# Kernel optimization log

Measured on AMD Instinct MI355X. Metric: run time of the kernel, lower is better.

## Reference

```python
import jax, jax.numpy as jnp
import numpy as np

R = 7            # radius
STRIDE = 2       # downsample_factor
K_SIDE = 2 * R + 1   # 15 -> K = 225 neighbors


def setup_inputs() -> dict:
    key = jax.random.key(0)
    B, H, W = 8, 512, 512
    # integer segment labels in [0, 64), stored as float32
    segments = jax.random.randint(key, (B, 1, H, W), 0, 64).astype(jnp.float32)
    return {"segments": segments}


def _local_equality_adj(segments):
    # segments: [B, 1, H_full, W_full]
    seg = segments[..., ::STRIDE, ::STRIDE]          # [B, 1, H, W]
    B, _, H, W = seg.shape
    x = seg[:, 0]                                    # [B, H, W]
    # zero-pad borders by R (unfold-style neighborhood extraction)
    padded = jnp.pad(x, ((0, 0), (R, R), (R, R)))    # [B, H+2R, W+2R]
    offs = jnp.arange(K_SIDE)
    dy, dx = jnp.meshgrid(offs, offs, indexing="ij")
    dy = dy.reshape(-1)                              # [K]
    dx = dx.reshape(-1)                              # [K]

    def gather(dy_i, dx_i):
        return jax.lax.dynamic_slice(padded, (0, dy_i, dx_i), (B, H, W))

    neighbors = jax.vmap(gather)(dy, dx)             # [K, B, H, W]
    neighbors = jnp.transpose(neighbors, (1, 0, 2, 3))  # [B, K, H, W]
    # broadcast equality: center [B,1,H,W] vs neighbors [B,K,H,W]
    adj = (seg == neighbors).astype(jnp.float32)     # [B, K, H, W]
    return adj


def reference(segments):
    return _local_equality_adj(segments)
```

## Files before the change

### kernel.cpp

```cpp
#include <hip/hip_runtime.h>


#define RAD 7
#define KS 15
#define HW 256
#define IN_W 512
#define TILE_W (HW + 2 * RAD)
#define TILE_PITCH 272
#define PLANE (HW * HW)

typedef float vf4 __attribute__((ext_vector_type(4)));

__global__ __launch_bounds__(256) void adj_kernel(const float* __restrict__ in,
                                                  float* __restrict__ out) {
    __shared__ float smem[KS][TILE_PITCH];

    const int y   = blockIdx.x;
    const int b   = blockIdx.y;
    const int tid = threadIdx.x;

    const float* inb = in + (size_t)b * (IN_W * IN_W);

    #pragma unroll
    for (int r = 0; r < KS; ++r) {
        const int gy = y - RAD + r;
        for (int c = tid; c < TILE_PITCH; c += 256) {
            const int gx = c - RAD;
            float v = 0.0f;
            if ((unsigned)gy < HW && (unsigned)gx < HW) {
                v = inb[(size_t)(2 * gy) * IN_W + 2 * gx];
            }
            smem[r][c] = v;
        }
    }
    __syncthreads();

    const int wv   = tid >> 6;
    const int lane = tid & 63;
    const int x    = lane * 4;

    const float s0 = smem[RAD][x + RAD + 0];
    const float s1 = smem[RAD][x + RAD + 1];
    const float s2 = smem[RAD][x + RAD + 2];
    const float s3 = smem[RAD][x + RAD + 3];

    float* base = out + (size_t)b * (KS * KS * (size_t)PLANE) + (size_t)y * HW + x;

    for (int r = wv; r < KS; r += 4) {
        const float* rowp = &smem[r][x];
        vf4 w0 = *(const vf4*)(rowp + 0);
        vf4 w1 = *(const vf4*)(rowp + 4);
        vf4 w2 = *(const vf4*)(rowp + 8);
        vf4 w3 = *(const vf4*)(rowp + 12);
        vf4 w4 = *(const vf4*)(rowp + 16);
        float win[20] = { w0.x, w0.y, w0.z, w0.w,
                          w1.x, w1.y, w1.z, w1.w,
                          w2.x, w2.y, w2.z, w2.w,
                          w3.x, w3.y, w3.z, w3.w,
                          w4.x, w4.y, w4.z, w4.w };
        float* op = base + (size_t)(r * KS) * PLANE;
        #pragma unroll
        for (int dc = 0; dc < KS; ++dc) {
            vf4 v;
            v.x = (s0 == win[dc + 0]) ? 1.0f : 0.0f;
            v.y = (s1 == win[dc + 1]) ? 1.0f : 0.0f;
            v.z = (s2 == win[dc + 2]) ? 1.0f : 0.0f;
            v.w = (s3 == win[dc + 3]) ? 1.0f : 0.0f;
            __builtin_nontemporal_store(v, (vf4*)op);
            op += PLANE;
        }
    }
}

extern "C" void kernel_launch(void* const* d_in, const int* in_sizes, int n_in,
                              void* d_out, int out_size, void* d_ws, size_t ws_size,
                              hipStream_t stream) {
    const float* segments = (const float*)d_in[0];
    float* out = (float*)d_out;
    dim3 grid(HW, 8);
    dim3 block(256);
    adj_kernel<<<grid, block, 0, stream>>>(segments, out);
}
```

Before: 463.0 us.

## Split into padded downsample pass and per-plane output-contiguous comparison kernel

```diff
diff --git a/kernel.cpp b/kernel.cpp
--- a/kernel.cpp
+++ b/kernel.cpp
@@ -5,70 +5,100 @@
 #define KS 15
 #define HW 256
 #define IN_W 512
-#define TILE_W (HW + 2 * RAD)
-#define TILE_PITCH 272
 #define PLANE (HW * HW)
+#define WSROWS 270
+#define WSPITCH 272
+#define WSPLANE (WSROWS * WSPITCH)
+#define WS_BYTES ((size_t)8 * WSPLANE * 4)
 
 typedef float vf4 __attribute__((ext_vector_type(4)));
 
-__global__ __launch_bounds__(256) void adj_kernel(const float* __restrict__ in,
+__global__ __launch_bounds__(256) void downsample_pad(const float* __restrict__ in,
+                                                      float* __restrict__ ws) {
+    int t = blockIdx.x * 256 + threadIdx.x;
+    const int N = 8 * WSPLANE;
+    if (t >= N) return;
+    int xx   = t % WSPITCH;
+    int rest = t / WSPITCH;
+    int yy   = rest % WSROWS;
+    int b    = rest / WSROWS;
+    int gy = yy - RAD;
+    int gx = xx - 8;
+    float v = 0.0f;
+    if ((unsigned)gy < HW && (unsigned)gx < HW) {
+        v = in[(size_t)b * (IN_W * IN_W) + (size_t)(2 * gy) * IN_W + 2 * gx];
+    }
+    ws[t] = v;
+}
+
+__global__ __launch_bounds__(256) void adj_planes(const float* __restrict__ ws,
                                                   float* __restrict__ out) {
-    __shared__ float smem[KS][TILE_PITCH];
+    const int bx = blockIdx.x;
+    const int p  = bx >> 2;
+    const int y0 = (bx & 3) * 64;
+    const int b  = blockIdx.y;
+    const int dy = p / KS;
+    const int dx = p - dy * KS;
 
-    const int y   = blockIdx.x;
-    const int b   = blockIdx.y;
-    const int tid = threadIdx.x;
-
-    const float* inb = in + (size_t)b * (IN_W * IN_W);
-
-    #pragma unroll
-    for (int r = 0; r < KS; ++r) {
-        const int gy = y - RAD + r;
-        for (int c = tid; c < TILE_PITCH; c += 256) {
-            const int gx = c - RAD;
-            float v = 0.0f;
-            if ((unsigned)gy < HW && (unsigned)gx < HW) {
-                v = inb[(size_t)(2 * gy) * IN_W + 2 * gx];
-            }
-            smem[r][c] = v;
-        }
-    }
-    __syncthreads();
-
+    const int tid  = threadIdx.x;
     const int wv   = tid >> 6;
     const int lane = tid & 63;
     const int x    = lane * 4;
 
-    const float s0 = smem[RAD][x + RAD + 0];
-    const float s1 = smem[RAD][x + RAD + 1];
-    const float s2 = smem[RAD][x + RAD + 2];
-    const float s3 = smem[RAD][x + RAD + 3];
+    const float* wsb = ws + (size_t)b * WSPLANE;
+    float* ob = out + ((size_t)(b * (KS * KS) + p)) * PLANE
+                    + (size_t)y0 * HW + x;
 
-    float* base = out + (size_t)b * (KS * KS * (size_t)PLANE) + (size_t)y * HW + x;
+    for (int yi = wv; yi < 64; yi += 4) {
+        const int y = y0 + yi;
+        const vf4 own = *(const vf4*)(wsb + (size_t)(y + RAD) * WSPITCH + 8 + x);
+        const float* np = wsb + (size_t)(y + dy) * WSPITCH + (x + dx + 1);
+        const float n0 = np[0], n1 = np[1], n2 = np[2], n3 = np[3];
+        vf4 v;
+        v.x = (own.x == n0) ? 1.0f : 0.0f;
+        v.y = (own.y == n1) ? 1.0f : 0.0f;
+        v.z = (own.z == n2) ? 1.0f : 0.0f;
+        v.w = (own.w == n3) ? 1.0f : 0.0f;
+        __builtin_nontemporal_store(v, (vf4*)(ob + (size_t)yi * HW));
+    }
+}
 
-    for (int r = wv; r < KS; r += 4) {
-        const float* rowp = &smem[r][x];
-        vf4 w0 = *(const vf4*)(rowp + 0);
-        vf4 w1 = *(const vf4*)(rowp + 4);
-        vf4 w2 = *(const vf4*)(rowp + 8);
-        vf4 w3 = *(const vf4*)(rowp + 12);
-        vf4 w4 = *(const vf4*)(rowp + 16);
-        float win[20] = { w0.x, w0.y, w0.z, w0.w,
-                          w1.x, w1.y, w1.z, w1.w,
-                          w2.x, w2.y, w2.z, w2.w,
-                          w3.x, w3.y, w3.z, w3.w,
-                          w4.x, w4.y, w4.z, w4.w };
-        float* op = base + (size_t)(r * KS) * PLANE;
+__global__ __launch_bounds__(256) void adj_planes_direct(const float* __restrict__ in,
+                                                         float* __restrict__ out) {
+    const int bx = blockIdx.x;
+    const int p  = bx >> 2;
+    const int y0 = (bx & 3) * 64;
+    const int b  = blockIdx.y;
+    const int dy = p / KS;
+    const int dx = p - dy * KS;
+
+    const int tid  = threadIdx.x;
+    const int wv   = tid >> 6;
+    const int lane = tid & 63;
+    const int x    = lane * 4;
+
+    const float* inb = in + (size_t)b * (IN_W * IN_W);
+    float* ob = out + ((size_t)(b * (KS * KS) + p)) * PLANE
+                    + (size_t)y0 * HW + x;
+
+    for (int yi = wv; yi < 64; yi += 4) {
+        const int y  = y0 + yi;
+        const int ny = y + dy - RAD;
+        const bool yok = (unsigned)ny < HW;
+        const float* own_row = inb + (size_t)(2 * y) * IN_W;
+        const float* nb_row  = inb + (size_t)(2 * (yok ? ny : 0)) * IN_W;
+        vf4 v;
         #pragma unroll
-        for (int dc = 0; dc < KS; ++dc) {
-            vf4 v;
-            v.x = (s0 == win[dc + 0]) ? 1.0f : 0.0f;
-            v.y = (s1 == win[dc + 1]) ? 1.0f : 0.0f;
-            v.z = (s2 == win[dc + 2]) ? 1.0f : 0.0f;
-            v.w = (s3 == win[dc + 3]) ? 1.0f : 0.0f;
-            __builtin_nontemporal_store(v, (vf4*)op);
-            op += PLANE;
+        for (int k = 0; k < 4; ++k) {
+            const float s = own_row[2 * (x + k)];
+            const int nx = x + k + dx - RAD;
+            float n = 0.0f;
+            if (yok && (unsigned)nx < HW) n = nb_row[2 * nx];
+            const float r = (s == n) ? 1.0f : 0.0f;
+            if (k == 0) v.x = r; else if (k == 1) v.y = r;
+            else if (k == 2) v.z = r; else v.w = r;
         }
+        __builtin_nontemporal_store(v, (vf4*)(ob + (size_t)yi * HW));
     }
 }
 
@@ -77,7 +107,13 @@
                               hipStream_t stream) {
     const float* segments = (const float*)d_in[0];
     float* out = (float*)d_out;
-    dim3 grid(HW, 8);
-    dim3 block(256);
-    adj_kernel<<<grid, block, 0, stream>>>(segments, out);
+
+    if (d_ws != nullptr && ws_size >= WS_BYTES) {
+        float* ws = (float*)d_ws;
+        const int N = 8 * WSPLANE;
+        downsample_pad<<<dim3((N + 255) / 256), dim3(256), 0, stream>>>(segments, ws);
+        adj_planes<<<dim3(KS * KS * 4, 8), dim3(256), 0, stream>>>(ws, out);
+    } else {
+        adj_planes_direct<<<dim3(KS * KS * 4, 8), dim3(256), 0, stream>>>(segments, out);
+    }
 }
```

After: 463.9 us. About the same (+0.2%).

## Parallelize over neighbor offsets with direct global reads instead of shared-memory tile

Applied to the files above, without the earlier changes.

```diff
diff --git a/kernel.cpp b/kernel.cpp
--- a/kernel.cpp
+++ b/kernel.cpp
@@ -5,70 +5,55 @@
 #define KS 15
 #define HW 256
 #define IN_W 512
-#define TILE_W (HW + 2 * RAD)
-#define TILE_PITCH 272
 #define PLANE (HW * HW)
 
 typedef float vf4 __attribute__((ext_vector_type(4)));
 
-__global__ __launch_bounds__(256) void adj_kernel(const float* __restrict__ in,
+__global__ __launch_bounds__(256) void adj_direct(const float* __restrict__ in,
                                                   float* __restrict__ out) {
-    __shared__ float smem[KS][TILE_PITCH];
+    const int p  = blockIdx.x;
+    const int y0 = blockIdx.y * 64;
+    const int b  = blockIdx.z;
+    const int dy = p / KS;
+    const int dx = p - dy * KS;
 
-    const int y   = blockIdx.x;
-    const int b   = blockIdx.y;
-    const int tid = threadIdx.x;
-
-    const float* inb = in + (size_t)b * (IN_W * IN_W);
-
-    #pragma unroll
-    for (int r = 0; r < KS; ++r) {
-        const int gy = y - RAD + r;
-        for (int c = tid; c < TILE_PITCH; c += 256) {
-            const int gx = c - RAD;
-            float v = 0.0f;
-            if ((unsigned)gy < HW && (unsigned)gx < HW) {
-                v = inb[(size_t)(2 * gy) * IN_W + 2 * gx];
-            }
-            smem[r][c] = v;
-        }
-    }
-    __syncthreads();
-
+    const int tid  = threadIdx.x;
     const int wv   = tid >> 6;
     const int lane = tid & 63;
     const int x    = lane * 4;
 
-    const float s0 = smem[RAD][x + RAD + 0];
-    const float s1 = smem[RAD][x + RAD + 1];
-    const float s2 = smem[RAD][x + RAD + 2];
-    const float s3 = smem[RAD][x + RAD + 3];
+    const float* inb = in + (size_t)b * (IN_W * IN_W);
+    float* ob = out + ((size_t)(b * (KS * KS) + p)) * PLANE
+                    + (size_t)y0 * HW + x;
 
-    float* base = out + (size_t)b * (KS * KS * (size_t)PLANE) + (size_t)y * HW + x;
+    const int nx0 = x + dx - RAD;
 
-    for (int r = wv; r < KS; r += 4) {
-        const float* rowp = &smem[r][x];
-        vf4 w0 = *(const vf4*)(rowp + 0);
-        vf4 w1 = *(const vf4*)(rowp + 4);
-        vf4 w2 = *(const vf4*)(rowp + 8);
-        vf4 w3 = *(const vf4*)(rowp + 12);
-        vf4 w4 = *(const vf4*)(rowp + 16);
-        float win[20] = { w0.x, w0.y, w0.z, w0.w,
-                          w1.x, w1.y, w1.z, w1.w,
-                          w2.x, w2.y, w2.z, w2.w,
-                          w3.x, w3.y, w3.z, w3.w,
-                          w4.x, w4.y, w4.z, w4.w };
-        float* op = base + (size_t)(r * KS) * PLANE;
+    for (int yi = wv; yi < 64; yi += 4) {
+        const int y  = y0 + yi;
+        const int ny = y + dy - RAD;
+        const bool yok = (unsigned)ny < (unsigned)HW;
+
+        const float* orow = inb + (size_t)(2 * y) * IN_W + 2 * x;
+        const vf4 o0 = *(const vf4*)(orow);
+        const vf4 o1 = *(const vf4*)(orow + 4);
+        const float s0 = o0.x, s1 = o0.z, s2 = o1.x, s3 = o1.z;
+
+        const float* nrow = inb + (size_t)(2 * (yok ? ny : 0)) * IN_W;
+        float n[4];
         #pragma unroll
-        for (int dc = 0; dc < KS; ++dc) {
-            vf4 v;
-            v.x = (s0 == win[dc + 0]) ? 1.0f : 0.0f;
-            v.y = (s1 == win[dc + 1]) ? 1.0f : 0.0f;
-            v.z = (s2 == win[dc + 2]) ? 1.0f : 0.0f;
-            v.w = (s3 == win[dc + 3]) ? 1.0f : 0.0f;
-            __builtin_nontemporal_store(v, (vf4*)op);
-            op += PLANE;
+        for (int k = 0; k < 4; ++k) {
+            const int c  = nx0 + k;
+            const bool ok = yok && ((unsigned)c < (unsigned)HW);
+            const float v = nrow[ok ? 2 * c : 0];
+            n[k] = ok ? v : 0.0f;
         }
+
+        vf4 r;
+        r.x = (s0 == n[0]) ? 1.0f : 0.0f;
+        r.y = (s1 == n[1]) ? 1.0f : 0.0f;
+        r.z = (s2 == n[2]) ? 1.0f : 0.0f;
+        r.w = (s3 == n[3]) ? 1.0f : 0.0f;
+        __builtin_nontemporal_store(r, (vf4*)(ob + (size_t)yi * HW));
     }
 }
 
@@ -77,7 +62,7 @@
                               hipStream_t stream) {
     const float* segments = (const float*)d_in[0];
     float* out = (float*)d_out;
-    dim3 grid(HW, 8);
+    dim3 grid(KS * KS, 4, 8);
     dim3 block(256);
-    adj_kernel<<<grid, block, 0, stream>>>(segments, out);
+    adj_direct<<<grid, block, 0, stream>>>(segments, out);
 }
```

New measurement: 615.4 us. 32.9% more time.
